# Kernel optimization log

Measured on AMD Instinct MI355X. Metric: run time of the kernel, lower is better.

Reference implementation:

```python
import jax, jax.numpy as jnp
import numpy as np

B, N, C_IN, C_OUT, K = 8, 1024, 64, 64, 4


def setup_inputs() -> dict:
    key = jax.random.key(0)
    k1, k2, k3 = jax.random.split(key, 3)
    x = jax.random.normal(k1, (B, N, C_IN), dtype=jnp.float32)
    # scaled-Laplacian-like matrix; 1/sqrt(N) scaling keeps Chebyshev recurrence stable
    L = jax.random.normal(k2, (B, N, N), dtype=jnp.float32) * (1.0 / np.sqrt(N))
    theta = jax.random.normal(k3, (K, C_IN, C_OUT), dtype=jnp.float32) * np.sqrt(2.0 / C_IN)
    return {"x": x, "L": L, "theta": theta}


def reference(x, L, theta):
    # Chebyshev recurrence applied directly to feature vectors:
    #   z0 = x, z1 = L x, z_k = 2 L z_{k-1} - z_{k-2}
    # out = sum_k z_k @ theta[k]  -- same math as materializing T_k(L),
    # since T_k(L) @ x obeys the same 3-term recurrence.
    k_orders = theta.shape[0]
    z_prev = x                      # [B,N,C]
    out = jnp.matmul(z_prev, theta[0])
    if k_orders > 1:
        z_curr = jnp.matmul(L, x)   # [B,N,C]
        out = out + jnp.matmul(z_curr, theta[1])
        for k in range(2, k_orders):
            z_next = 2.0 * jnp.matmul(L, z_curr) - z_prev
            out = out + jnp.matmul(z_next, theta[k])
            z_prev, z_curr = z_curr, z_next
    return out
```

## Files before the change

kernel.cpp:

```cpp
#include <hip/hip_runtime.h>
#include <cstdint>
#include <cstddef>


typedef __bf16 bf16;
typedef bf16 bf16x8 __attribute__((ext_vector_type(8)));
typedef float f32x4 __attribute__((ext_vector_type(4)));

#define MFMA_BF16(a, b, c) __builtin_amdgcn_mfma_f32_16x16x32_bf16((a), (b), (c), 0, 0, 0)
#define WAITV(n) asm volatile("s_waitcnt vmcnt(" #n ")" ::: "memory")

__device__ __forceinline__ void dma16(const void* g, void* l) {
    __builtin_amdgcn_global_load_lds(
        (const __attribute__((address_space(1))) unsigned int*)g,
        (__attribute__((address_space(3))) unsigned int*)l, 16, 0, 0);
}

__global__ __launch_bounds__(256) void prep_kernel(const float* __restrict__ x,
                                                   const float* __restrict__ theta,
                                                   const float* __restrict__ Lmat,
                                                   bf16* __restrict__ xT,
                                                   bf16* __restrict__ xb,
                                                   bf16* __restrict__ thT,
                                                   bf16* __restrict__ Lb)
{
    const int bid = blockIdx.x;
    const int t = threadIdx.x;

    if (bid >= 132) {
        constexpr int CHUNKS = (8 * 1024 * 1024) / 8;
        const int stride = (1156 - 132) * 256;
        for (int idx = (bid - 132) * 256 + t; idx < CHUNKS; idx += stride) {
            f32x4 v0 = ((const f32x4*)Lmat)[2 * idx];
            f32x4 v1 = ((const f32x4*)Lmat)[2 * idx + 1];
            bf16x8 q;
#pragma unroll
            for (int i = 0; i < 4; ++i) { q[i] = (bf16)v0[i]; q[4 + i] = (bf16)v1[i]; }
            ((bf16x8*)Lb)[idx] = q;
        }
        return;
    }

    __shared__ bf16 tile[64][72];
    const int r = t >> 2;
    const int c0 = (t & 3) << 4;
    const float* src;
    bf16* dstT;
    int dst_ld;
    const bool isx = bid < 128;
    int b = 0, n0 = 0;
    if (isx) {
        b = bid >> 4; n0 = (bid & 15) << 6;
        src = x + (size_t)(b * 1024 + n0) * 64;
        dstT = xT + (size_t)b * 64 * 1024 + n0;
        dst_ld = 1024;
    } else {
        const int k = bid - 128;
        src = theta + (size_t)k * 4096;
        dstT = thT + (size_t)k * 4096;
        dst_ld = 64;
    }

    bf16x8 row0, row1;
#pragma unroll
    for (int j = 0; j < 16; j += 4) {
        f32x4 v = *reinterpret_cast<const f32x4*>(src + r * 64 + c0 + j);
#pragma unroll
        for (int i = 0; i < 4; ++i) {
            bf16 q = (bf16)v[i];
            tile[r][c0 + j + i] = q;
            if (j + i < 8) row0[j + i] = q; else row1[j + i - 8] = q;
        }
    }
    if (isx) {
        bf16* xr = xb + (size_t)(b * 1024 + n0 + r) * 64 + c0;
        *reinterpret_cast<bf16x8*>(xr) = row0;
        *reinterpret_cast<bf16x8*>(xr + 8) = row1;
    }
    __syncthreads();
    bf16x8 o0, o1;
#pragma unroll
    for (int j = 0; j < 8; ++j) { o0[j] = tile[c0 + j][r]; o1[j] = tile[c0 + 8 + j][r]; }
    *reinterpret_cast<bf16x8*>(dstT + (size_t)r * dst_ld + c0) = o0;
    *reinterpret_cast<bf16x8*>(dstT + (size_t)r * dst_ld + c0 + 8) = o1;
}

template <int STAGE>
__global__ __launch_bounds__(512) void stage_kernel(
    const bf16* __restrict__ Lb,
    const bf16* __restrict__ xb,
    const bf16* __restrict__ zinT,
    const bf16* __restrict__ zprevT,
    const bf16* __restrict__ thT,
    bf16* __restrict__ zoutT,
    float* __restrict__ out)
{
    constexpr int D = 5, T = 16, KS = 64, LSTG = 12288;
    __shared__ __align__(16) unsigned char smem[D * LSTG];

    const int bid = blockIdx.x;
    const int b  = bid >> 5;
    const int m0 = (bid & 31) << 5;
    const int t  = threadIdx.x;
    const int w  = t >> 6;
    const int l  = t & 63;
    const int l15 = l & 15;
    const int lg  = l >> 4;
    const int wq  = w & 3;
    const int h   = w >> 2;

    const bf16* Lrb = Lb + ((size_t)(b * 1024 + m0)) * 1024;
    const bf16* zb  = zinT + (size_t)b * 64 * 1024;

    const int Lg = (w << 5) + (l & 31);
    const int Lrow = Lg >> 3, Lslot = Lg & 7;
    const bf16* Lsrc = Lrb + (size_t)Lrow * 1024 + (Lslot ^ (Lrow & 7)) * 8;
    const int Zg = (w << 6) + l;
    const int Zch = Zg >> 3;
    const bf16* Zsrc = zb + (size_t)Zch * 1024 + ((Zg & 7) ^ (Zch & 7)) * 8;

    auto issue = [&](int k0, unsigned char* bufb) {
        dma16(Zsrc + k0, bufb + 4096 + (w << 10));
        if (l < 32)
            dma16(Lsrc + k0, bufb + (w << 9));
    };

    f32x4 acc = {0.f, 0.f, 0.f, 0.f};

    auto computeStep = [&](const unsigned char* bufb) {
        const bf16* Ll = (const bf16*)bufb;
        const bf16* Zl = (const bf16*)(bufb + 4096);
        const int chan = (wq << 4) + l15;
        const int sA = chan & 7;
        bf16x8 a0 = *(const bf16x8*)(Zl + (((chan << 3) + (lg ^ sA)) << 3));
        bf16x8 a1 = *(const bf16x8*)(Zl + (((chan << 3) + ((4 + lg) ^ sA)) << 3));
        const int mrow = (h << 4) + l15;
        const int sB = mrow & 7;
        bf16x8 b0 = *(const bf16x8*)(Ll + (((mrow << 3) + (lg ^ sB)) << 3));
        bf16x8 b1 = *(const bf16x8*)(Ll + (((mrow << 3) + ((4 + lg) ^ sB)) << 3));
        acc = MFMA_BF16(a0, b0, acc);
        acc = MFMA_BF16(a1, b1, acc);
    };

#pragma unroll
    for (int s = 0; s < D - 1; ++s)
        issue(s * KS, smem + s * LSTG);

#pragma unroll
    for (int tt = 0; tt < T; ++tt) {
        const int rem = ((T - tt) < (D - 1) ? (T - tt) : (D - 1)) - 1;
        if (rem >= 3)      WAITV(6);
        else if (rem == 2) WAITV(4);
        else if (rem == 1) WAITV(2);
        else               WAITV(0);
        __builtin_amdgcn_sched_barrier(0);
        __builtin_amdgcn_s_barrier();
        __builtin_amdgcn_sched_barrier(0);
        computeStep(smem + (tt % D) * LSTG);
        if (tt + D - 1 < T)
            issue((tt + D - 1) * KS, smem + ((tt + D - 1) % D) * LSTG);
    }

    bf16 (*zbuf)[72] = (bf16(*)[72])(smem + LSTG);
    const int cr   = (wq << 4) + (lg << 2);
    const int mcol = m0 + (h << 4) + l15;
    const float alpha = (STAGE == 1) ? 1.0f : 2.0f;
    float zv[4];
#pragma unroll
    for (int r = 0; r < 4; ++r) {
        float zp = 0.f;
        if constexpr (STAGE >= 2)
            zp = (float)zprevT[(size_t)(b * 64 + cr + r) * 1024 + mcol];
        zv[r] = alpha * acc[r] - zp;
    }
    if constexpr (STAGE <= 2) {
#pragma unroll
        for (int r = 0; r < 4; ++r)
            zoutT[(size_t)(b * 64 + cr + r) * 1024 + mcol] = (bf16)zv[r];
    }
#pragma unroll
    for (int r = 0; r < 4; ++r)
        zbuf[(h << 4) + l15][cr + r] = (bf16)zv[r];
    __syncthreads();

    const int o = (wq << 4) + l15;
    const int mrowA = m0 + (h << 4) + l15;
    f32x4 oacc;
    if constexpr (STAGE == 1) {
        oacc = (f32x4){0.f, 0.f, 0.f, 0.f};
#pragma unroll
        for (int ck = 0; ck < 2; ++ck) {
            bf16x8 ax = *reinterpret_cast<const bf16x8*>(
                xb + (size_t)(b * 1024 + mrowA) * 64 + ck * 32 + lg * 8);
            bf16x8 bt = *reinterpret_cast<const bf16x8*>(
                thT + (size_t)o * 64 + ck * 32 + lg * 8);
            oacc = MFMA_BF16(ax, bt, oacc);
        }
    } else {
#pragma unroll
        for (int r = 0; r < 4; ++r)
            oacc[r] = out[(size_t)(b * 1024 + m0 + (h << 4) + lg * 4 + r) * 64 + o];
    }
    constexpr int KTH = (STAGE == 1) ? 1 : STAGE;
#pragma unroll
    for (int ck = 0; ck < 2; ++ck) {
        bf16x8 az = *reinterpret_cast<const bf16x8*>(
            &zbuf[(h << 4) + l15][ck * 32 + lg * 8]);
        bf16x8 bt = *reinterpret_cast<const bf16x8*>(
            thT + (size_t)(KTH * 64 + o) * 64 + ck * 32 + lg * 8);
        oacc = MFMA_BF16(az, bt, oacc);
    }
#pragma unroll
    for (int r = 0; r < 4; ++r)
        out[(size_t)(b * 1024 + m0 + (h << 4) + lg * 4 + r) * 64 + o] = oacc[r];
}

extern "C" void kernel_launch(void* const* d_in, const int* in_sizes, int n_in,
                              void* d_out, int out_size, void* d_ws, size_t ws_size,
                              hipStream_t stream)
{
    const float* x  = (const float*)d_in[0];
    const float* L  = (const float*)d_in[1];
    const float* th = (const float*)d_in[2];
    float* out = (float*)d_out;

    bf16* xT  = (bf16*)d_ws;
    bf16* xb  = xT  + (size_t)8 * 64 * 1024;
    bf16* z1T = xb  + (size_t)8 * 64 * 1024;
    bf16* z2T = z1T + (size_t)8 * 64 * 1024;
    bf16* thT = z2T + (size_t)8 * 64 * 1024;
    bf16* Lb  = thT + (size_t)4 * 64 * 64;

    prep_kernel<<<dim3(1156), dim3(256), 0, stream>>>(x, th, L, xT, xb, thT, Lb);
    stage_kernel<1><<<dim3(256), dim3(512), 0, stream>>>(Lb, xb, xT, nullptr, thT, z1T, out);
    stage_kernel<2><<<dim3(256), dim3(512), 0, stream>>>(Lb, xb, z1T, xT, thT, z2T, out);
    stage_kernel<3><<<dim3(256), dim3(512), 0, stream>>>(Lb, xb, z2T, z1T, thT, nullptr, out);
}
```

Measured before the change: 99.73 us.

## Fuse fp32-to-bf16 conversion of L into the first Chebyshev stage kernel

Stage 1 now DMA-loads fp32 L tiles directly into shared memory, converts them to bf16 in registers for the MFMA, and writes the bf16 copy of L for later stages. The prep kernel no longer converts L, removing a separate full pass over L and one read of the bf16 copy. Stage 1 pipeline depth drops from 5 to 4 buffers because fp32 tiles are larger, and the kernel adds conversion ALU work and global stores inside the main loop.

```diff
diff --git a/kernel.cpp b/kernel.cpp
--- a/kernel.cpp
+++ b/kernel.cpp
@@ -18,30 +18,13 @@
 
 __global__ __launch_bounds__(256) void prep_kernel(const float* __restrict__ x,
                                                    const float* __restrict__ theta,
-                                                   const float* __restrict__ Lmat,
                                                    bf16* __restrict__ xT,
                                                    bf16* __restrict__ xb,
-                                                   bf16* __restrict__ thT,
-                                                   bf16* __restrict__ Lb)
+                                                   bf16* __restrict__ thT)
 {
+    __shared__ bf16 tile[64][72];
     const int bid = blockIdx.x;
     const int t = threadIdx.x;
-
-    if (bid >= 132) {
-        constexpr int CHUNKS = (8 * 1024 * 1024) / 8;
-        const int stride = (1156 - 132) * 256;
-        for (int idx = (bid - 132) * 256 + t; idx < CHUNKS; idx += stride) {
-            f32x4 v0 = ((const f32x4*)Lmat)[2 * idx];
-            f32x4 v1 = ((const f32x4*)Lmat)[2 * idx + 1];
-            bf16x8 q;
-#pragma unroll
-            for (int i = 0; i < 4; ++i) { q[i] = (bf16)v0[i]; q[4 + i] = (bf16)v1[i]; }
-            ((bf16x8*)Lb)[idx] = q;
-        }
-        return;
-    }
-
-    __shared__ bf16 tile[64][72];
     const int r = t >> 2;
     const int c0 = (t & 3) << 4;
     const float* src;
@@ -85,6 +68,132 @@
     *reinterpret_cast<bf16x8*>(dstT + (size_t)r * dst_ld + c0 + 8) = o1;
 }
 
+__global__ __launch_bounds__(512) void stage1_kernel(
+    const float* __restrict__ Lmat,
+    const bf16* __restrict__ xb,
+    const bf16* __restrict__ zinT,
+    const bf16* __restrict__ thT,
+    bf16* __restrict__ Lb,
+    bf16* __restrict__ zoutT,
+    float* __restrict__ out)
+{
+    constexpr int D = 4, T = 16, KS = 64, LSTG = 16384;
+    __shared__ __align__(16) unsigned char smem[D * LSTG];
+
+    const int bid = blockIdx.x;
+    const int b  = bid >> 5;
+    const int m0 = (bid & 31) << 5;
+    const int t  = threadIdx.x;
+    const int w  = t >> 6;
+    const int l  = t & 63;
+    const int l15 = l & 15;
+    const int lg  = l >> 4;
+    const int wq  = w & 3;
+    const int h   = w >> 2;
+
+    const float* Lrb = Lmat + ((size_t)(b * 1024 + m0)) * 1024;
+    const bf16*  zb  = zinT + (size_t)b * 64 * 1024;
+
+    const int Lrow = t >> 4, Lslot = t & 15;
+    const float* Lsrc = Lrb + (size_t)Lrow * 1024 + ((Lslot ^ (Lrow & 7)) << 2);
+    const int Zg = (w << 6) + l;
+    const int Zch = Zg >> 3;
+    const bf16* Zsrc = zb + (size_t)Zch * 1024 + ((Zg & 7) ^ (Zch & 7)) * 8;
+
+    auto issue = [&](int k0, unsigned char* bufb) {
+        dma16(Lsrc + k0, bufb + (w << 10));
+        dma16(Zsrc + k0, bufb + 8192 + (w << 10));
+    };
+
+    f32x4 acc = {0.f, 0.f, 0.f, 0.f};
+    const int mrow = (h << 4) + l15;
+    bf16* Lbrow = Lb + (size_t)(b * 1024 + m0 + mrow) * 1024;
+
+    auto computeStep = [&](const unsigned char* bufb, int k0) {
+        const float* Ll = (const float*)bufb;
+        const bf16*  Zl = (const bf16*)(bufb + 8192);
+        const int chan = (wq << 4) + l15;
+        const int sA = chan & 7;
+        bf16x8 a0 = *(const bf16x8*)(Zl + (((chan << 3) + (lg ^ sA)) << 3));
+        bf16x8 a1 = *(const bf16x8*)(Zl + (((chan << 3) + ((4 + lg) ^ sA)) << 3));
+        const int sB = mrow & 7;
+        const float* Lr = Ll + (mrow << 6);
+        f32x4 u0 = *(const f32x4*)(Lr + ((((lg << 1) | 0) ^ sB) << 2));
+        f32x4 u1 = *(const f32x4*)(Lr + ((((lg << 1) | 1) ^ sB) << 2));
+        f32x4 v0 = *(const f32x4*)(Lr + (((8 + ((lg << 1) | 0)) ^ sB) << 2));
+        f32x4 v1 = *(const f32x4*)(Lr + (((8 + ((lg << 1) | 1)) ^ sB) << 2));
+        bf16x8 b0, b1;
+#pragma unroll
+        for (int j = 0; j < 4; ++j) {
+            b0[j] = (bf16)u0[j]; b0[4 + j] = (bf16)u1[j];
+            b1[j] = (bf16)v0[j]; b1[4 + j] = (bf16)v1[j];
+        }
+        if (wq == 0) {
+            *reinterpret_cast<bf16x8*>(Lbrow + k0 + (lg << 3))      = b0;
+            *reinterpret_cast<bf16x8*>(Lbrow + k0 + 32 + (lg << 3)) = b1;
+        }
+        acc = MFMA_BF16(a0, b0, acc);
+        acc = MFMA_BF16(a1, b1, acc);
+    };
+
+#pragma unroll
+    for (int s = 0; s < D - 1; ++s)
+        issue(s * KS, smem + s * LSTG);
+
+#pragma unroll
+    for (int tt = 0; tt < T; ++tt) {
+        const int rem = ((T - tt) < (D - 1) ? (T - tt) : (D - 1)) - 1;
+        if (rem >= 2)      WAITV(4);
+        else if (rem == 1) WAITV(2);
+        else               WAITV(0);
+        __builtin_amdgcn_sched_barrier(0);
+        __builtin_amdgcn_s_barrier();
+        __builtin_amdgcn_sched_barrier(0);
+        computeStep(smem + (tt % D) * LSTG, tt * KS);
+        __builtin_amdgcn_sched_barrier(0);
+        if (tt + D - 1 < T)
+            issue((tt + D - 1) * KS, smem + ((tt + D - 1) % D) * LSTG);
+        __builtin_amdgcn_sched_barrier(0);
+    }
+
+    bf16 (*zbuf)[72] = (bf16(*)[72])(smem + LSTG);
+    const int cr   = (wq << 4) + (lg << 2);
+    const int mcol = m0 + (h << 4) + l15;
+    float zv[4];
+#pragma unroll
+    for (int r = 0; r < 4; ++r) zv[r] = acc[r];
+#pragma unroll
+    for (int r = 0; r < 4; ++r)
+        zoutT[(size_t)(b * 64 + cr + r) * 1024 + mcol] = (bf16)zv[r];
+#pragma unroll
+    for (int r = 0; r < 4; ++r)
+        zbuf[(h << 4) + l15][cr + r] = (bf16)zv[r];
+    __syncthreads();
+
+    const int o = (wq << 4) + l15;
+    const int mrowA = m0 + (h << 4) + l15;
+    f32x4 oacc = {0.f, 0.f, 0.f, 0.f};
+#pragma unroll
+    for (int ck = 0; ck < 2; ++ck) {
+        bf16x8 ax = *reinterpret_cast<const bf16x8*>(
+            xb + (size_t)(b * 1024 + mrowA) * 64 + ck * 32 + lg * 8);
+        bf16x8 bt = *reinterpret_cast<const bf16x8*>(
+            thT + (size_t)o * 64 + ck * 32 + lg * 8);
+        oacc = MFMA_BF16(ax, bt, oacc);
+    }
+#pragma unroll
+    for (int ck = 0; ck < 2; ++ck) {
+        bf16x8 az = *reinterpret_cast<const bf16x8*>(
+            &zbuf[(h << 4) + l15][ck * 32 + lg * 8]);
+        bf16x8 bt = *reinterpret_cast<const bf16x8*>(
+            thT + (size_t)(64 + o) * 64 + ck * 32 + lg * 8);
+        oacc = MFMA_BF16(az, bt, oacc);
+    }
+#pragma unroll
+    for (int r = 0; r < 4; ++r)
+        out[(size_t)(b * 1024 + m0 + (h << 4) + lg * 4 + r) * 64 + o] = oacc[r];
+}
+
 template <int STAGE>
 __global__ __launch_bounds__(512) void stage_kernel(
     const bf16* __restrict__ Lb,
@@ -164,14 +273,11 @@
     bf16 (*zbuf)[72] = (bf16(*)[72])(smem + LSTG);
     const int cr   = (wq << 4) + (lg << 2);
     const int mcol = m0 + (h << 4) + l15;
-    const float alpha = (STAGE == 1) ? 1.0f : 2.0f;
     float zv[4];
 #pragma unroll
     for (int r = 0; r < 4; ++r) {
-        float zp = 0.f;
-        if constexpr (STAGE >= 2)
-            zp = (float)zprevT[(size_t)(b * 64 + cr + r) * 1024 + mcol];
-        zv[r] = alpha * acc[r] - zp;
+        float zp = (float)zprevT[(size_t)(b * 64 + cr + r) * 1024 + mcol];
+        zv[r] = 2.0f * acc[r] - zp;
     }
     if constexpr (STAGE <= 2) {
 #pragma unroll
@@ -184,24 +290,11 @@
     __syncthreads();
 
     const int o = (wq << 4) + l15;
-    const int mrowA = m0 + (h << 4) + l15;
     f32x4 oacc;
-    if constexpr (STAGE == 1) {
-        oacc = (f32x4){0.f, 0.f, 0.f, 0.f};
-#pragma unroll
-        for (int ck = 0; ck < 2; ++ck) {
-            bf16x8 ax = *reinterpret_cast<const bf16x8*>(
-                xb + (size_t)(b * 1024 + mrowA) * 64 + ck * 32 + lg * 8);
-            bf16x8 bt = *reinterpret_cast<const bf16x8*>(
-                thT + (size_t)o * 64 + ck * 32 + lg * 8);
-            oacc = MFMA_BF16(ax, bt, oacc);
-        }
-    } else {
-#pragma unroll
-        for (int r = 0; r < 4; ++r)
-            oacc[r] = out[(size_t)(b * 1024 + m0 + (h << 4) + lg * 4 + r) * 64 + o];
-    }
-    constexpr int KTH = (STAGE == 1) ? 1 : STAGE;
+#pragma unroll
+    for (int r = 0; r < 4; ++r)
+        oacc[r] = out[(size_t)(b * 1024 + m0 + (h << 4) + lg * 4 + r) * 64 + o];
+    constexpr int KTH = STAGE;
 #pragma unroll
     for (int ck = 0; ck < 2; ++ck) {
         bf16x8 az = *reinterpret_cast<const bf16x8*>(
@@ -231,8 +324,8 @@
     bf16* thT = z2T + (size_t)8 * 64 * 1024;
     bf16* Lb  = thT + (size_t)4 * 64 * 64;
 
-    prep_kernel<<<dim3(1156), dim3(256), 0, stream>>>(x, th, L, xT, xb, thT, Lb);
-    stage_kernel<1><<<dim3(256), dim3(512), 0, stream>>>(Lb, xb, xT, nullptr, thT, z1T, out);
+    prep_kernel<<<dim3(132), dim3(256), 0, stream>>>(x, th, xT, xb, thT);
+    stage1_kernel<<<dim3(256), dim3(512), 0, stream>>>(L, xb, xT, thT, Lb, z1T, out);
     stage_kernel<2><<<dim3(256), dim3(512), 0, stream>>>(Lb, xb, z1T, xT, thT, z2T, out);
     stage_kernel<3><<<dim3(256), dim3(512), 0, stream>>>(Lb, xb, z2T, z1T, thT, nullptr, out);
 }
```

Measured after the change: 101.4 us. About the same (+1.7%).
